# Kernel tuning notes

Measured on AMD Instinct MI355X. Metric: run time of the kernel, lower is better.

## Reference

```python
import jax, jax.numpy as jnp
import numpy as np

B = 128          # batch size
N_KG = 500       # KG vertices
N = N_KG + 2     # + sensor node + zero target node
D = 1024         # embed_dim (hard-coded in forward)
H = 256          # gnn_hidden
E = 4000         # edges
EPS = 1e-5


def setup_inputs() -> dict:
    key = jax.random.key(0)
    ks = jax.random.split(key, 8)
    return {
        "sensor_batch": jax.random.normal(ks[0], (B, D), jnp.float32),
        "base_vertices": jax.random.normal(ks[1], (N_KG, D), jnp.float32),
        "edge_index": jax.random.randint(ks[2], (2, E), 0, N, jnp.int64),
        "W1": jax.random.normal(ks[3], (D, H), jnp.float32) * (1.0 / np.sqrt(D)),
        "b1": jnp.zeros((H,), jnp.float32),
        "gamma1": jnp.ones((H,), jnp.float32),
        "beta1": jnp.zeros((H,), jnp.float32),
        "W2": jax.random.normal(ks[4], (H, H), jnp.float32) * (1.0 / np.sqrt(H)),
        "b2": jnp.zeros((H,), jnp.float32),
        "gamma2": jnp.ones((H,), jnp.float32),
        "beta2": jnp.zeros((H,), jnp.float32),
        "W3": jax.random.normal(ks[5], (H, H), jnp.float32) * (1.0 / np.sqrt(H)),
        "b3": jnp.zeros((H,), jnp.float32),
        "gamma3": jnp.ones((H,), jnp.float32),
        "beta3": jnp.zeros((H,), jnp.float32),
    }


def _gcn_norm(edge_index):
    # add self loops, symmetric normalization D^{-1/2} A D^{-1/2}
    loops = jnp.arange(N, dtype=edge_index.dtype)
    src = jnp.concatenate([edge_index[0], loops])
    dst = jnp.concatenate([edge_index[1], loops])
    deg = jnp.zeros((N,), jnp.float32).at[dst].add(1.0)
    dinv = jnp.where(deg > 0, jax.lax.rsqrt(deg), 0.0)
    norm = dinv[src] * dinv[dst]   # [E+N]
    return src, dst, norm


def _gcn_conv(x, W, b, src, dst, norm):
    # x: [B, N, F_in] -> [B, N, F_out]
    h = jnp.einsum('bnf,fh->bnh', x, W)
    msg = h[:, src, :] * norm[None, :, None]            # gather + scale
    out = jnp.zeros_like(h).at[:, dst, :].add(msg)      # scatter-add
    return out + b


def _bn_elu(x, gamma, beta):
    # BatchNorm1d over flattened (B*N, H) in training mode, then ELU
    Bn, Nn, Hh = x.shape
    xf = x.reshape(Bn * Nn, Hh)
    mean = jnp.mean(xf, axis=0)
    var = jnp.mean(jnp.square(xf - mean), axis=0)  # biased, as in torch BN fwd
    y = (xf - mean) * jax.lax.rsqrt(var + EPS) * gamma + beta
    return jax.nn.elu(y).reshape(Bn, Nn, Hh)


def reference(sensor_batch, base_vertices, edge_index,
              W1, b1, gamma1, beta1,
              W2, b2, gamma2, beta2,
              W3, b3, gamma3, beta3):
    Bn = sensor_batch.shape[0]
    # x = [base_vertices; sensor_input; zeros] per batch element -> [B, N, D]
    base = jnp.broadcast_to(base_vertices[None], (Bn, N_KG, D))
    zeros = jnp.zeros((Bn, 1, D), sensor_batch.dtype)
    x = jnp.concatenate([base, sensor_batch[:, None, :], zeros], axis=1)

    src, dst, norm = _gcn_norm(edge_index)
    x = _bn_elu(_gcn_conv(x, W1, b1, src, dst, norm), gamma1, beta1)
    x = _bn_elu(_gcn_conv(x, W2, b2, src, dst, norm), gamma2, beta2)
    x = _bn_elu(_gcn_conv(x, W3, b3, src, dst, norm), gamma3, beta3)
    return x
```

## Files before the change

kernel.cpp:

```cpp
#include <hip/hip_runtime.h>
#include <cstdint>
#include <cstddef>

#define NNODES 502
#define NKG    500
#define NPAD   512
#define NEDGE  4000
#define NET    4502
#define BB     128
#define DD     1024
#define HH     256
#define MROWS  (BB*NNODES)
#define MT     65536
#define MCAT   628
#define EPITCH 136

typedef short short8 __attribute__((ext_vector_type(8)));
typedef float f32x4  __attribute__((ext_vector_type(4)));

__device__ __forceinline__ unsigned short f2bf(float f) {
  union { float f; unsigned int u; } v; v.f = f;
  unsigned int r = v.u + 0x7fffu + ((v.u >> 16) & 1u);
  return (unsigned short)(r >> 16);
}

__device__ __forceinline__ float bf2f(unsigned short u) {
  union { unsigned int u; float f; } v; v.u = ((unsigned int)u) << 16;
  return v.f;
}

__device__ __forceinline__ float elu(float y) {
  return (y > 0.f) ? y : (__expf(y) - 1.f);
}

__device__ __forceinline__ void stage16(const void* g, void* l) {
  __builtin_amdgcn_global_load_lds((__attribute__((address_space(1))) void*)g,
                                   (__attribute__((address_space(3))) void*)l, 16, 0, 0);
}

__device__ __forceinline__ void mfma16(f32x4& c, short8 a, short8 b) {
  asm volatile("v_mfma_f32_16x16x32_bf16 %0, %1, %2, %0" : "+v"(c) : "v"(a), "v"(b));
}

__device__ inline void get_edge(const int* __restrict__ e, int i, int i64mode,
                                int& src, int& dst) {
  if (i < NEDGE) {
    if (i64mode) { src = e[2*i]; dst = e[2*NEDGE + 2*i]; }
    else         { src = e[i];   dst = e[NEDGE + i]; }
  } else {
    src = dst = i - NEDGE;
  }
  src = min(max(src, 0), NNODES-1);
  dst = min(max(dst, 0), NNODES-1);
}

__device__ __forceinline__ int detect_mode(const int* __restrict__ e) {
  __shared__ int sflag;
  if (threadIdx.x == 0) sflag = 0;
  __syncthreads();
  if (e[2*threadIdx.x + 1] != 0) atomicOr(&sflag, 1);
  __syncthreads();
  return sflag == 0;
}

__global__ void deg_kernel(const int* __restrict__ e, int* __restrict__ deg) {
  int i64 = detect_mode(e);
  int i = blockIdx.x*256 + threadIdx.x;
  if (i >= NET) return;
  int src, dst; get_edge(e, i, i64, src, dst);
  atomicAdd(&deg[dst], 1);
}

__global__ void scan_kernel(const int* __restrict__ deg, float* __restrict__ dinv,
                            int* __restrict__ rp, int* __restrict__ cursor) {
  __shared__ int s[512];
  int t = threadIdx.x;
  int cnt = (t < NNODES) ? deg[t] : 0;
  s[t] = cnt;
  if (t < NNODES) dinv[t] = rsqrtf((float)cnt);
  __syncthreads();
  for (int off = 1; off < 512; off <<= 1) {
    int v = (t >= off) ? s[t-off] : 0;
    __syncthreads();
    s[t] += v;
    __syncthreads();
  }
  if (t == 0) rp[0] = 0;
  if (t < NNODES) { rp[t+1] = s[t]; cursor[t] = s[t] - cnt; }
}

__global__ void fillsdf_kernel(const int* __restrict__ e, const float* __restrict__ dinv,
                               int* __restrict__ cursor, int* __restrict__ colA,
                               float* __restrict__ valA, float* __restrict__ Sdf) {
  int i64 = detect_mode(e);
  int i = blockIdx.x*256 + threadIdx.x;
  if (i >= NET) return;
  int src, dst; get_edge(e, i, i64, src, dst);
  float v = dinv[src] * dinv[dst];
  int pos = atomicAdd(&cursor[dst], 1);
  colA[pos] = src;
  valA[pos] = v;
  atomicAdd(&Sdf[dst*NPAD + src], v);
}

__global__ void sdcvt_kernel(const float* __restrict__ Sdf, unsigned short* __restrict__ Sd) {
  int i = blockIdx.x*256 + threadIdx.x;
  Sd[i] = f2bf(Sdf[i]);
}

__global__ __launch_bounds__(256) void prep_kernel(
    const float* __restrict__ W1, const float* __restrict__ W2, const float* __restrict__ W3,
    const float* __restrict__ base, const float* __restrict__ sensor,
    unsigned short* __restrict__ Wt1, unsigned short* __restrict__ Wt2,
    unsigned short* __restrict__ Wt3, unsigned short* __restrict__ Xp1,
    float* __restrict__ hcatz) {
  int bid = blockIdx.x, tid = threadIdx.x;
  if (bid < 512) {
    const float* W = (bid & 256) ? W3 : W2;
    unsigned short* Wt = (bid & 256) ? Wt3 : Wt2;
    int n = bid & 255;
    Wt[n*HH + tid] = f2bf(W[(size_t)tid*HH + n]);
  } else if (bid < 768) {
    int n = bid - 512;
    for (int k = tid; k < DD; k += 256)
      Wt1[n*DD + k] = f2bf(W1[(size_t)k*HH + n]);
  } else if (bid < 1408) {
    int i = (bid - 768)*256 + tid;
    int r = i >> 8, c = (i & 255) * 4;
    float4 v = make_float4(0.f, 0.f, 0.f, 0.f);
    if (r < NKG) v = *(const float4*)&base[(size_t)r*DD + c];
    else if (r < MCAT) v = *(const float4*)&sensor[(size_t)(r-NKG)*DD + c];
    union { unsigned short u[4]; uint2 d; } p;
    p.u[0]=f2bf(v.x); p.u[1]=f2bf(v.y); p.u[2]=f2bf(v.z); p.u[3]=f2bf(v.w);
    *(uint2*)&Xp1[(size_t)r*DD + c] = p.d;
  } else {
    hcatz[(bid - 1408)*256 + tid] = 0.f;
  }
}

__global__ __launch_bounds__(256) void gemm1m_kernel(
    const unsigned short* __restrict__ Ag,
    const unsigned short* __restrict__ Bg,
    float* __restrict__ C) {
  __shared__ unsigned short As[128*32];
  __shared__ unsigned short Bs[128*32];
  int tid = threadIdx.x;
  int wave = tid >> 6, lane = tid & 63;
  int l15 = lane & 15, quad = lane >> 4;
  int wm = (wave & 1) * 64, wn = (wave >> 1) * 64;
  int row0 = blockIdx.y * 128, col0 = blockIdx.x * 128;
  int kbase = blockIdx.z * 256;
  f32x4 acc[4][4] = {};
  for (int k0 = kbase; k0 < kbase + 256; k0 += 32) {
#pragma unroll
    for (int q = 0; q < 2; ++q) {
      int c = wave*128 + q*64 + lane;
      stage16(Ag + (size_t)(row0 + (c>>2))*DD + k0 + (c&3)*8, As + c*8);
      stage16(Bg + (size_t)(col0 + (c>>2))*DD + k0 + (c&3)*8, Bs + c*8);
    }
    __syncthreads();
    short8 af[4], bfv[4];
#pragma unroll
    for (int i = 0; i < 4; ++i) {
      af[i]  = *(const short8*)(As + (wm + i*16 + l15)*32 + quad*8);
      bfv[i] = *(const short8*)(Bs + (wn + i*16 + l15)*32 + quad*8);
    }
#pragma unroll
    for (int mi = 0; mi < 4; ++mi)
#pragma unroll
      for (int ni = 0; ni < 4; ++ni)
        mfma16(acc[mi][ni], af[mi], bfv[ni]);
    __syncthreads();
  }
  asm volatile("s_nop 7\n\ts_nop 7" ::);
#pragma unroll
  for (int ni = 0; ni < 4; ++ni) {
    int n = col0 + wn + ni*16 + l15;
#pragma unroll
    for (int mi = 0; mi < 4; ++mi) {
      int m = row0 + wm + mi*16 + quad*4;
#pragma unroll
      for (int r = 0; r < 4; ++r)
        if (m + r < MCAT) atomicAdd(&C[(size_t)(m+r)*HH + n], acc[mi][ni][r]);
    }
  }
}

__global__ void ac_kernel(const int* __restrict__ rp, const int* __restrict__ colA,
                          const float* __restrict__ valA, const float* __restrict__ hcat,
                          float* __restrict__ Abuf, float* __restrict__ cbuf) {
  int n = blockIdx.x, h = threadIdx.x;
  int s = rp[n], e = rp[n+1];
  float acc = 0.f, cacc = 0.f;
  for (int t = s; t < e; ++t) {
    int cl = colA[t]; float v = valA[t];
    if (cl < NKG) acc += v * hcat[cl*HH + h];
    else if (cl == NKG) cacc += v;
  }
  Abuf[n*HH + h] = acc;
  if (h == 0) cbuf[n] = cacc;
}

__global__ __launch_bounds__(256) void bn1n_kernel(
    const float* __restrict__ Abuf, const float* __restrict__ cbuf,
    const float* __restrict__ hcat,
    float* __restrict__ sA1, float* __restrict__ sAA1, float* __restrict__ sAc1,
    float* __restrict__ scp, float* __restrict__ ssA, float* __restrict__ sssA) {
  int bid = blockIdx.x, h = threadIdx.x;
  if (bid < 32) {
    int n0 = bid*16, n1 = min(n0+16, NNODES);
    float sA = 0, sAA = 0, sAc = 0, sc = 0, scc = 0;
    for (int n = n0; n < n1; ++n) {
      float a = Abuf[n*HH + h]; float cn = cbuf[n];
      sA += a; sAA += a*a; sAc += a*cn; sc += cn; scc += cn*cn;
    }
    atomicAdd(&sA1[h], sA); atomicAdd(&sAA1[h], sAA); atomicAdd(&sAc1[h], sAc);
    if (h == 0) { atomicAdd(&scp[0], sc); atomicAdd(&scp[1], scc); }
  } else {
    int b0 = (bid-32)*16;
    float ss = 0, sss = 0;
    for (int b = b0; b < b0+16; ++b) {
      float v = hcat[(size_t)(NKG + b)*HH + h]; ss += v; sss += v*v;
    }
    atomicAdd(&ssA[h], ss); atomicAdd(&sssA[h], sss);
  }
}

__global__ void fin1_kernel(const float* __restrict__ sA1, const float* __restrict__ sAA1,
                            const float* __restrict__ sAc1, const float* __restrict__ scp,
                            const float* __restrict__ ssA, const float* __restrict__ sssA,
                            const float* __restrict__ gamma, const float* __restrict__ beta,
                            float* __restrict__ scale, float* __restrict__ shift) {
  int h = threadIdx.x;
  float sA = sA1[h], sAA = sAA1[h], sAc = sAc1[h];
  float sc = scp[0], scc = scp[1];
  float ss = ssA[h], sss = sssA[h];
  const float cnt = (float)MROWS;
  float mean = ((float)BB * sA + sc*ss) / cnt;
  float msq  = ((float)BB * sAA + 2.f*sAc*ss + scc*sss) / cnt;
  float var  = msq - mean*mean;
  float scl  = gamma[h] * rsqrtf(var + 1e-5f);
  scale[h] = scl; shift[h] = beta[h] - mean*scl;
}

__global__ __launch_bounds__(256) void x2_kernel(
    const float* __restrict__ Abuf, const float* __restrict__ cbuf,
    const float* __restrict__ hcat, const float* __restrict__ scale,
    const float* __restrict__ shift, unsigned short* __restrict__ Xb) {
  int idx = blockIdx.x*256 + threadIdx.x;
  int row = idx >> 6, h0 = (idx & 63)*4;
  int b = row >> 9, n = row & (NPAD-1);
  union { unsigned short u[4]; uint2 d; } p;
  p.d = make_uint2(0,0);
  if (n < NNODES) {
    float4 a  = *(const float4*)(Abuf + n*HH + h0);
    float4 s  = *(const float4*)(hcat + (size_t)(NKG + b)*HH + h0);
    float4 sc = *(const float4*)(scale + h0);
    float4 sh = *(const float4*)(shift + h0);
    float cn = cbuf[n];
    p.u[0] = f2bf(elu((a.x + cn*s.x)*sc.x + sh.x));
    p.u[1] = f2bf(elu((a.y + cn*s.y)*sc.y + sh.y));
    p.u[2] = f2bf(elu((a.z + cn*s.z)*sc.z + sh.z));
    p.u[3] = f2bf(elu((a.w + cn*s.w)*sc.w + sh.w));
  }
  *(uint2*)(Xb + (size_t)row*HH + h0) = p.d;
}

template<int FBN>
__global__ __launch_bounds__(256) void gemmT3_kernel(
    const unsigned short* __restrict__ Ag,
    const unsigned short* __restrict__ Bg,
    const float* __restrict__ sums, const float* __restrict__ ssqs,
    const float* __restrict__ gamma, const float* __restrict__ beta,
    unsigned short* __restrict__ Tt) {
  __shared__ __align__(16) unsigned short smem[36864];
  __shared__ float sclL[256], shfL[256];
  unsigned short* As = smem;
  unsigned short* Bs = smem + 12288;
  int tid = threadIdx.x;
  int wave = tid >> 6, lane = tid & 63;
  int l15 = lane & 15, quad = lane >> 4;
  int wm = (wave & 1) * 64;
  int wnh = wave >> 1;
  int row0 = blockIdx.x * 128;
  if (FBN) {
    float mean = sums[tid] * (1.f/(float)MROWS);
    float var  = ssqs[tid] * (1.f/(float)MROWS) - mean*mean;
    float s = gamma[tid] * rsqrtf(var + 1e-5f);
    sclL[tid] = s; shfL[tid] = beta[tid] - mean*s;
    __syncthreads();
  }
  int c0 = tid, c1 = 256 + tid;
  int r0 = c0 >> 2, o0 = (c0 & 3) * 8;
  int r1 = c1 >> 2, o1 = (c1 & 3) * 8;
  const unsigned short* A0 = Ag + (size_t)(row0 + r0)*HH + o0;
  const unsigned short* A1 = Ag + (size_t)(row0 + r1)*HH + o1;

  auto XF = [&](uint4 v, int kk) -> uint4 {
    union { unsigned short u[8]; uint4 d; } va, pa;
    va.d = v;
#pragma unroll
    for (int s = 0; s < 8; ++s)
      pa.u[s] = f2bf(elu(bf2f(va.u[s])*sclL[kk+s] + shfL[kk+s]));
    return pa.d;
  };
  auto STAGE_B = [&](int kn, int buf) {
#pragma unroll
    for (int q = 0; q < 4; ++q) {
      int c = q*256 + tid;
      int rr = c >> 2, j = (c & 3)*8;
      stage16(Bg + (size_t)rr*HH + kn + j, Bs + buf*8192 + c*8);
    }
  };

  f32x4 acc[4][8] = {};
  if (FBN) {
    uint4 p00 = *(const uint4*)(A0);
    uint4 p01 = *(const uint4*)(A1);
    uint4 p10 = *(const uint4*)(A0 + 32);
    uint4 p11 = *(const uint4*)(A1 + 32);
    STAGE_B(0, 0);
    STAGE_B(32, 1);
    *(uint4*)(As + c0*8)        = XF(p00, o0);
    *(uint4*)(As + c1*8)        = XF(p01, o1);
    *(uint4*)(As + 4096 + c0*8) = XF(p10, 32 + o0);
    *(uint4*)(As + 4096 + c1*8) = XF(p11, 32 + o1);
    asm volatile("s_waitcnt lgkmcnt(0)" ::: "memory");
  } else {
    stage16(A0, As + c0*8);
    stage16(A1, As + c1*8);
    STAGE_B(0, 0);
    stage16(A0 + 32, As + 4096 + c0*8);
    stage16(A1 + 32, As + 4096 + c1*8);
    STAGE_B(32, 1);
  }
  uint4 na0, na1;
#pragma unroll
  for (int t = 0; t < 8; ++t) {
    int cur = t % 3;
    int nxt2 = (t + 2) % 3;
    if (FBN) {
      if (t >= 1 && t <= 6) {
        na0 = *(const uint4*)(A0 + (t+1)*32);
        na1 = *(const uint4*)(A1 + (t+1)*32);
      }
      if (t < 6) STAGE_B((t+2)*32, nxt2);
      if (t == 0)      asm volatile("s_waitcnt vmcnt(8)"  ::: "memory");
      else if (t <= 5) asm volatile("s_waitcnt vmcnt(10)" ::: "memory");
      else if (t == 6) asm volatile("s_waitcnt vmcnt(6)"  ::: "memory");
      else             asm volatile("s_waitcnt vmcnt(0)"  ::: "memory");
    } else {
      if (t < 6) {
        stage16(A0 + (t+2)*32, As + nxt2*4096 + c0*8);
        stage16(A1 + (t+2)*32, As + nxt2*4096 + c1*8);
        STAGE_B((t+2)*32, nxt2);
        asm volatile("s_waitcnt vmcnt(12)" ::: "memory");
      } else if (t == 6) {
        asm volatile("s_waitcnt vmcnt(6)" ::: "memory");
      } else {
        asm volatile("s_waitcnt vmcnt(0)" ::: "memory");
      }
    }
    __builtin_amdgcn_s_barrier();
    __builtin_amdgcn_sched_barrier(0);
    short8 af[4], bfv[8];
#pragma unroll
    for (int i = 0; i < 4; ++i)
      af[i] = *(const short8*)(As + cur*4096 + (wm + i*16 + l15)*32 + quad*8);
#pragma unroll
    for (int i = 0; i < 8; ++i)
      bfv[i] = *(const short8*)(Bs + cur*8192 + (wnh*128 + i*16 + l15)*32 + quad*8);
#pragma unroll
    for (int mi = 0; mi < 4; ++mi)
#pragma unroll
      for (int ni = 0; ni < 8; ++ni)
        mfma16(acc[mi][ni], af[mi], bfv[ni]);
    if (FBN && t >= 1 && t <= 6) {
      int nb = (t + 1) % 3;
      int kk = (t + 1) * 32;
      *(uint4*)(As + nb*4096 + c0*8) = XF(na0, kk + o0);
      *(uint4*)(As + nb*4096 + c1*8) = XF(na1, kk + o1);
      asm volatile("s_waitcnt lgkmcnt(0)" ::: "memory");
    }
    __builtin_amdgcn_sched_barrier(0);
    __builtin_amdgcn_s_barrier();
  }
  asm volatile("s_nop 7\n\ts_nop 7" ::);
  int moff = (tid & 15)*8;
#pragma unroll
  for (int nh = 0; nh < 2; ++nh) {
    if (wnh == nh) {
#pragma unroll
      for (int ni = 0; ni < 8; ++ni) {
        int nl = ni*16 + l15;
#pragma unroll
        for (int mi = 0; mi < 4; ++mi) {
          int ml = wm + mi*16 + quad*4;
#pragma unroll
          for (int r = 0; r < 4; ++r)
            smem[nl*EPITCH + ml + r] = f2bf(acc[mi][ni][r]);
        }
      }
    }
    __syncthreads();
#pragma unroll
    for (int j = 0; j < 8; ++j) {
      int nr = (tid >> 4) + j*16;
      uint4 d = *(const uint4*)(smem + nr*EPITCH + moff);
      *(uint4*)(Tt + (size_t)(nh*128 + nr)*MT + row0 + moff) = d;
    }
    __syncthreads();
  }
}

__global__ __launch_bounds__(256) void gemmS2_kernel(
    const unsigned short* __restrict__ Sd,
    const unsigned short* __restrict__ Tt,
    unsigned short* __restrict__ Xbo,
    float* __restrict__ sums, float* __restrict__ ssqs) {
  __shared__ __align__(16) unsigned short smem[36864];
  unsigned short* As = smem;
  unsigned short* Bs = smem + 12288;
  int tid = threadIdx.x;
  int wave = tid >> 6, lane = tid & 63;
  int l15 = lane & 15, quad = lane >> 4;
  int wm = (wave & 1) * 64, wn = (wave >> 1) * 64;
  int id = blockIdx.x;
  int xcd = id & 7;
  int w = id >> 3;
  int y = w & 3;
  int g = (w >> 2) * 8 + xcd;
  int x = g >> 6;
  int b = (g & 63) * 2;
  int row0 = y * 128, col0 = x * 128;
  const unsigned short* Abase = Sd + (size_t)row0*NPAD;
  const unsigned short* Bbase = Tt + (size_t)col0*MT + (size_t)b*NPAD;
  int c0 = tid, c1 = 256 + tid;
  int r0 = c0 >> 2, o0 = (c0 & 3) * 8;
  int r1 = c1 >> 2, o1 = (c1 & 3) * 8;

  f32x4 acc[2][4][4] = {};
  auto STAGE = [&](int kn, int buf) {
    stage16(Abase + (size_t)r0*NPAD + kn + o0, As + buf*4096 + c0*8);
    stage16(Abase + (size_t)r1*NPAD + kn + o1, As + buf*4096 + c1*8);
#pragma unroll
    for (int q = 0; q < 4; ++q) {
      int c = q*256 + tid;
      int bb = c >> 9, cc = c & 511;
      int rr = cc >> 2, j = (cc & 3)*8;
      stage16(Bbase + (size_t)rr*MT + bb*NPAD + kn + j, Bs + buf*8192 + c*8);
    }
  };
  STAGE(0, 0);
  STAGE(32, 1);
  for (int t = 0; t < 16; ++t) {
    int cur = t % 3;
    if (t < 14) {
      STAGE((t+2)*32, (t+2) % 3);
      asm volatile("s_waitcnt vmcnt(12)" ::: "memory");
    } else if (t == 14) {
      asm volatile("s_waitcnt vmcnt(6)" ::: "memory");
    } else {
      asm volatile("s_waitcnt vmcnt(0)" ::: "memory");
    }
    __builtin_amdgcn_s_barrier();
    __builtin_amdgcn_sched_barrier(0);
    short8 af[4], bfv[2][4];
#pragma unroll
    for (int i = 0; i < 4; ++i)
      af[i] = *(const short8*)(As + cur*4096 + (wm + i*16 + l15)*32 + quad*8);
#pragma unroll
    for (int bb = 0; bb < 2; ++bb)
#pragma unroll
      for (int i = 0; i < 4; ++i)
        bfv[bb][i] = *(const short8*)(Bs + cur*8192 + bb*4096 + (wn + i*16 + l15)*32 + quad*8);
#pragma unroll
    for (int bb = 0; bb < 2; ++bb)
#pragma unroll
      for (int mi = 0; mi < 4; ++mi)
#pragma unroll
        for (int ni = 0; ni < 4; ++ni)
          mfma16(acc[bb][mi][ni], af[mi], bfv[bb][ni]);
    __builtin_amdgcn_sched_barrier(0);
    __builtin_amdgcn_s_barrier();
  }
  asm volatile("s_nop 7\n\ts_nop 7" ::);
  float ps[4] = {0,0,0,0}, pq[4] = {0,0,0,0};
#pragma unroll
  for (int bb = 0; bb < 2; ++bb)
#pragma unroll
    for (int ni = 0; ni < 4; ++ni)
#pragma unroll
      for (int mi = 0; mi < 4; ++mi)
#pragma unroll
        for (int r = 0; r < 4; ++r) {
          float v = acc[bb][mi][ni][r];
          ps[ni] += v; pq[ni] += v*v;
        }
  int noff = (tid & 15)*8;
#pragma unroll
  for (int bb = 0; bb < 2; ++bb) {
#pragma unroll
    for (int mi = 0; mi < 4; ++mi) {
      int ml = wm + mi*16 + quad*4;
#pragma unroll
      for (int ni = 0; ni < 4; ++ni) {
        int nl = wn + ni*16 + l15;
#pragma unroll
        for (int r = 0; r < 4; ++r)
          smem[(ml + r)*EPITCH + nl] = f2bf(acc[bb][mi][ni][r]);
      }
    }
    __syncthreads();
    unsigned short* Xrow = Xbo + (size_t)(b + bb)*NPAD*HH;
#pragma unroll
    for (int j = 0; j < 8; ++j) {
      int rr = (tid >> 4) + j*16;
      int node = row0 + rr;
      if (node < NNODES) {
        uint4 d = *(const uint4*)(smem + rr*EPITCH + noff);
        *(uint4*)(Xrow + (size_t)node*HH + col0 + noff) = d;
      }
    }
    __syncthreads();
  }
  float* red = (float*)smem;
  red[tid] = 0.f;
  __syncthreads();
#pragma unroll
  for (int ni = 0; ni < 4; ++ni) {
    int cl = wn + ni*16 + l15;
    atomicAdd(&red[cl], ps[ni]);
    atomicAdd(&red[128+cl], pq[ni]);
  }
  __syncthreads();
  if (tid < 128) atomicAdd(&sums[col0+tid], red[tid]);
  else atomicAdd(&ssqs[col0+tid-128], red[tid]);
}

__global__ void finalize_kernel(const float* __restrict__ sums, const float* __restrict__ ssqs,
                                const float* __restrict__ gamma, const float* __restrict__ beta,
                                float* __restrict__ scale, float* __restrict__ shift) {
  int h = threadIdx.x;
  const float cnt = (float)MROWS;
  float mean = sums[h] / cnt;
  float var  = ssqs[h] / cnt - mean*mean;
  float scl  = gamma[h] * rsqrtf(var + 1e-5f);
  scale[h] = scl; shift[h] = beta[h] - mean*scl;
}

__global__ __launch_bounds__(256) void bnout_kernel(
    const unsigned short* __restrict__ Xb, const float* __restrict__ scale,
    const float* __restrict__ shift, float* __restrict__ O) {
  int idx = blockIdx.x*256 + threadIdx.x;
  int row = idx >> 6, h0 = (idx & 63)*4;
  int b = row >> 9, n = row & (NPAD-1);
  if (n >= NNODES) return;
  union { unsigned short u[4]; uint2 d; } v;
  v.d = *(const uint2*)(Xb + (size_t)row*HH + h0);
  float4 sc = *(const float4*)(scale + h0);
  float4 sh = *(const float4*)(shift + h0);
  float4 o;
  o.x = elu(bf2f(v.u[0])*sc.x + sh.x);
  o.y = elu(bf2f(v.u[1])*sc.y + sh.y);
  o.z = elu(bf2f(v.u[2])*sc.z + sh.z);
  o.w = elu(bf2f(v.u[3])*sc.w + sh.w);
  *(float4*)(O + ((size_t)(b*NNODES + n)*HH + h0)) = o;
}

extern "C" void kernel_launch(void* const* d_in, const int* in_sizes, int n_in,
                              void* d_out, int out_size, void* d_ws, size_t ws_size,
                              hipStream_t stream) {
  const float* sensor = (const float*)d_in[0];
  const float* base   = (const float*)d_in[1];
  const int*   eidx   = (const int*)d_in[2];
  const float* W1 = (const float*)d_in[3];
  const float* g1 = (const float*)d_in[5];
  const float* be1= (const float*)d_in[6];
  const float* W2 = (const float*)d_in[7];
  const float* g2 = (const float*)d_in[9];
  const float* be2= (const float*)d_in[10];
  const float* W3 = (const float*)d_in[11];
  const float* g3 = (const float*)d_in[13];
  const float* be3= (const float*)d_in[14];

  char* ws = (char*)d_ws;
  int*   deg    = (int*)(ws + 0);
  float* sum2   = (float*)(ws + 2048);
  float* ssq2   = (float*)(ws + 3072);
  float* sum3   = (float*)(ws + 4096);
  float* ssq3   = (float*)(ws + 5120);
  float* cbuf   = (float*)(ws + 6144);
  int*   cursor = (int*)(ws + 8192);
  float* sA1    = (float*)(ws + 10496);
  float* sAA1   = (float*)(ws + 11520);
  float* sAc1   = (float*)(ws + 12544);
  float* scp    = (float*)(ws + 13568);
  float* ssA    = (float*)(ws + 13824);
  float* sssA   = (float*)(ws + 14848);
  float* dinv   = (float*)(ws + 16384);
  int*   rp     = (int*)(ws + 18432);
  int*   colA   = (int*)(ws + 20480);
  float* valA   = (float*)(ws + 40960);
  float* scale1 = (float*)(ws + 61440);
  float* shift1 = (float*)(ws + 62464);
  float* scale3 = (float*)(ws + 65536);
  float* shift3 = (float*)(ws + 66560);
  float* Abuf   = (float*)(ws + 67584);
  float* hcat   = (float*)(ws + 581632);
  unsigned short* Wt2 = (unsigned short*)(ws + 1224704);
  unsigned short* Wt3 = (unsigned short*)(ws + 1355776);
  unsigned short* Sd  = (unsigned short*)(ws + 1486848);
  unsigned short* Xb  = (unsigned short*)(ws + 2011136);
  unsigned short* Tt  = (unsigned short*)(ws + 35565568UL);
  unsigned short* Xp1 = (unsigned short*)(ws + 35565568UL);
  unsigned short* Wt1 = (unsigned short*)(ws + 35565568UL + 1310720);
  float* out = (float*)d_out;
  float* Sdf = (float*)d_out;

  hipMemsetAsync(ws, 0, 16384, stream);
  hipMemsetAsync(d_out, 0, NPAD*NPAD*4, stream);
  deg_kernel<<<(NET+255)/256, 256, 0, stream>>>(eidx, deg);
  scan_kernel<<<1, 512, 0, stream>>>(deg, dinv, rp, cursor);
  fillsdf_kernel<<<(NET+255)/256, 256, 0, stream>>>(eidx, dinv, cursor, colA, valA, Sdf);
  sdcvt_kernel<<<(NPAD*NPAD)/256, 256, 0, stream>>>(Sdf, Sd);
  prep_kernel<<<2036, 256, 0, stream>>>(W1, W2, W3, base, sensor, Wt1, Wt2, Wt3, Xp1, hcat);

  gemm1m_kernel<<<dim3(2, 5, 4), 256, 0, stream>>>(Xp1, Wt1, hcat);
  ac_kernel<<<NNODES, 256, 0, stream>>>(rp, colA, valA, hcat, Abuf, cbuf);
  bn1n_kernel<<<40, 256, 0, stream>>>(Abuf, cbuf, hcat, sA1, sAA1, sAc1, scp, ssA, sssA);
  fin1_kernel<<<1, 256, 0, stream>>>(sA1, sAA1, sAc1, scp, ssA, sssA, g1, be1, scale1, shift1);
  x2_kernel<<<(MT*64)/256, 256, 0, stream>>>(Abuf, cbuf, hcat, scale1, shift1, Xb);

  gemmT3_kernel<0><<<MT/128, 256, 0, stream>>>(Xb, Wt2, sum2, ssq2, g2, be2, Tt);
  gemmS2_kernel<<<512, 256, 0, stream>>>(Sd, Tt, Xb, sum2, ssq2);
  gemmT3_kernel<1><<<MT/128, 256, 0, stream>>>(Xb, Wt3, sum2, ssq2, g2, be2, Tt);
  gemmS2_kernel<<<512, 256, 0, stream>>>(Sd, Tt, Xb, sum3, ssq3);
  finalize_kernel<<<1, 256, 0, stream>>>(sum3, ssq3, g3, be3, scale3, shift3);
  bnout_kernel<<<(MT*64)/256, 256, 0, stream>>>(Xb, scale3, shift3, out);
}
```

Before: 289.0 us.

## Replace dense adjacency GEMM aggregation with sparse CSR gather kernel

The layer 2/3 aggregation switches from a dense bf16 512x512 normalized-adjacency matrix multiply (with a transposed H layout) to a CSR gather-accumulate kernel that reads neighbor rows of H directly. The dense adjacency build, its bf16 conversion and the related memset are dropped, and the feature GEMM now writes H row-major. This removes the dense GEMM's mostly-zero work, since there are only about 4500 nonzeros against 262k entries. The cost is irregular gathers, a 64-float per-thread accumulator that raises register pressure, and many shared-memory atomics for the BN statistics.

```diff
diff --git a/kernel.cpp b/kernel.cpp
--- a/kernel.cpp
+++ b/kernel.cpp
@@ -14,6 +14,7 @@
 #define MT     65536
 #define MCAT   628
 #define EPITCH 136
+#define EP2    264
 
 typedef short short8 __attribute__((ext_vector_type(8)));
 typedef float f32x4  __attribute__((ext_vector_type(4)));
@@ -89,23 +90,16 @@
   if (t < NNODES) { rp[t+1] = s[t]; cursor[t] = s[t] - cnt; }
 }
 
-__global__ void fillsdf_kernel(const int* __restrict__ e, const float* __restrict__ dinv,
-                               int* __restrict__ cursor, int* __restrict__ colA,
-                               float* __restrict__ valA, float* __restrict__ Sdf) {
+__global__ void fill_kernel(const int* __restrict__ e, const float* __restrict__ dinv,
+                            int* __restrict__ cursor, int* __restrict__ colA,
+                            float* __restrict__ valA) {
   int i64 = detect_mode(e);
   int i = blockIdx.x*256 + threadIdx.x;
   if (i >= NET) return;
   int src, dst; get_edge(e, i, i64, src, dst);
-  float v = dinv[src] * dinv[dst];
   int pos = atomicAdd(&cursor[dst], 1);
   colA[pos] = src;
-  valA[pos] = v;
-  atomicAdd(&Sdf[dst*NPAD + src], v);
-}
-
-__global__ void sdcvt_kernel(const float* __restrict__ Sdf, unsigned short* __restrict__ Sd) {
-  int i = blockIdx.x*256 + threadIdx.x;
-  Sd[i] = f2bf(Sdf[i]);
+  valA[pos] = dinv[src] * dinv[dst];
 }
 
 __global__ __launch_bounds__(256) void prep_kernel(
@@ -272,7 +266,7 @@
     const unsigned short* __restrict__ Bg,
     const float* __restrict__ sums, const float* __restrict__ ssqs,
     const float* __restrict__ gamma, const float* __restrict__ beta,
-    unsigned short* __restrict__ Tt) {
+    unsigned short* __restrict__ Hout) {
   __shared__ __align__(16) unsigned short smem[36864];
   __shared__ float sclL[256], shfL[256];
   unsigned short* As = smem;
@@ -386,156 +380,96 @@
     __builtin_amdgcn_s_barrier();
   }
   asm volatile("s_nop 7\n\ts_nop 7" ::);
-  int moff = (tid & 15)*8;
-#pragma unroll
-  for (int nh = 0; nh < 2; ++nh) {
-    if (wnh == nh) {
-#pragma unroll
-      for (int ni = 0; ni < 8; ++ni) {
-        int nl = ni*16 + l15;
-#pragma unroll
-        for (int mi = 0; mi < 4; ++mi) {
-          int ml = wm + mi*16 + quad*4;
-#pragma unroll
-          for (int r = 0; r < 4; ++r)
-            smem[nl*EPITCH + ml + r] = f2bf(acc[mi][ni][r]);
-        }
-      }
-    }
-    __syncthreads();
-#pragma unroll
-    for (int j = 0; j < 8; ++j) {
-      int nr = (tid >> 4) + j*16;
-      uint4 d = *(const uint4*)(smem + nr*EPITCH + moff);
-      *(uint4*)(Tt + (size_t)(nh*128 + nr)*MT + row0 + moff) = d;
-    }
-    __syncthreads();
-  }
-}
-
-__global__ __launch_bounds__(256) void gemmS2_kernel(
-    const unsigned short* __restrict__ Sd,
-    const unsigned short* __restrict__ Tt,
+#pragma unroll
+  for (int ni = 0; ni < 8; ++ni) {
+    int nl = wnh*128 + ni*16 + l15;
+#pragma unroll
+    for (int mi = 0; mi < 4; ++mi) {
+      int ml = wm + mi*16 + quad*4;
+#pragma unroll
+      for (int r = 0; r < 4; ++r)
+        smem[(ml + r)*EP2 + nl] = f2bf(acc[mi][ni][r]);
+    }
+  }
+  __syncthreads();
+  int colq = (tid & 31) * 8;
+  int rbase = tid >> 5;
+#pragma unroll
+  for (int j = 0; j < 16; ++j) {
+    int row = j*8 + rbase;
+    uint4 d = *(const uint4*)(smem + row*EP2 + colq);
+    *(uint4*)(Hout + (size_t)(row0 + row)*HH + colq) = d;
+  }
+}
+
+__global__ __launch_bounds__(256) void agg_kernel(
+    const int* __restrict__ rp, const int* __restrict__ colA,
+    const float* __restrict__ valA, const unsigned short* __restrict__ H,
     unsigned short* __restrict__ Xbo,
     float* __restrict__ sums, float* __restrict__ ssqs) {
-  __shared__ __align__(16) unsigned short smem[36864];
-  unsigned short* As = smem;
-  unsigned short* Bs = smem + 12288;
+  __shared__ float red[512];
+  int id = blockIdx.x;
+  int b = id & 127, chunk = id >> 7;
   int tid = threadIdx.x;
-  int wave = tid >> 6, lane = tid & 63;
-  int l15 = lane & 15, quad = lane >> 4;
-  int wm = (wave & 1) * 64, wn = (wave >> 1) * 64;
-  int id = blockIdx.x;
-  int xcd = id & 7;
-  int w = id >> 3;
-  int y = w & 3;
-  int g = (w >> 2) * 8 + xcd;
-  int x = g >> 6;
-  int b = (g & 63) * 2;
-  int row0 = y * 128, col0 = x * 128;
-  const unsigned short* Abase = Sd + (size_t)row0*NPAD;
-  const unsigned short* Bbase = Tt + (size_t)col0*MT + (size_t)b*NPAD;
-  int c0 = tid, c1 = 256 + tid;
-  int r0 = c0 >> 2, o0 = (c0 & 3) * 8;
-  int r1 = c1 >> 2, o1 = (c1 & 3) * 8;
-
-  f32x4 acc[2][4][4] = {};
-  auto STAGE = [&](int kn, int buf) {
-    stage16(Abase + (size_t)r0*NPAD + kn + o0, As + buf*4096 + c0*8);
-    stage16(Abase + (size_t)r1*NPAD + kn + o1, As + buf*4096 + c1*8);
-#pragma unroll
-    for (int q = 0; q < 4; ++q) {
-      int c = q*256 + tid;
-      int bb = c >> 9, cc = c & 511;
-      int rr = cc >> 2, j = (cc & 3)*8;
-      stage16(Bbase + (size_t)rr*MT + bb*NPAD + kn + j, Bs + buf*8192 + c*8);
-    }
-  };
-  STAGE(0, 0);
-  STAGE(32, 1);
-  for (int t = 0; t < 16; ++t) {
-    int cur = t % 3;
-    if (t < 14) {
-      STAGE((t+2)*32, (t+2) % 3);
-      asm volatile("s_waitcnt vmcnt(12)" ::: "memory");
-    } else if (t == 14) {
-      asm volatile("s_waitcnt vmcnt(6)" ::: "memory");
-    } else {
-      asm volatile("s_waitcnt vmcnt(0)" ::: "memory");
-    }
-    __builtin_amdgcn_s_barrier();
-    __builtin_amdgcn_sched_barrier(0);
-    short8 af[4], bfv[2][4];
-#pragma unroll
-    for (int i = 0; i < 4; ++i)
-      af[i] = *(const short8*)(As + cur*4096 + (wm + i*16 + l15)*32 + quad*8);
-#pragma unroll
-    for (int bb = 0; bb < 2; ++bb)
-#pragma unroll
-      for (int i = 0; i < 4; ++i)
-        bfv[bb][i] = *(const short8*)(Bs + cur*8192 + bb*4096 + (wn + i*16 + l15)*32 + quad*8);
-#pragma unroll
-    for (int bb = 0; bb < 2; ++bb)
-#pragma unroll
-      for (int mi = 0; mi < 4; ++mi)
-#pragma unroll
-        for (int ni = 0; ni < 4; ++ni)
-          mfma16(acc[bb][mi][ni], af[mi], bfv[bb][ni]);
-    __builtin_amdgcn_sched_barrier(0);
-    __builtin_amdgcn_s_barrier();
-  }
-  asm volatile("s_nop 7\n\ts_nop 7" ::);
-  float ps[4] = {0,0,0,0}, pq[4] = {0,0,0,0};
-#pragma unroll
-  for (int bb = 0; bb < 2; ++bb)
-#pragma unroll
-    for (int ni = 0; ni < 4; ++ni)
-#pragma unroll
-      for (int mi = 0; mi < 4; ++mi)
-#pragma unroll
-        for (int r = 0; r < 4; ++r) {
-          float v = acc[bb][mi][ni][r];
-          ps[ni] += v; pq[ni] += v*v;
-        }
-  int noff = (tid & 15)*8;
-#pragma unroll
-  for (int bb = 0; bb < 2; ++bb) {
-#pragma unroll
-    for (int mi = 0; mi < 4; ++mi) {
-      int ml = wm + mi*16 + quad*4;
-#pragma unroll
-      for (int ni = 0; ni < 4; ++ni) {
-        int nl = wn + ni*16 + l15;
-#pragma unroll
-        for (int r = 0; r < 4; ++r)
-          smem[(ml + r)*EPITCH + nl] = f2bf(acc[bb][mi][ni][r]);
+  int dst = chunk*64 + (tid >> 2);
+  int c0 = (tid & 3) * 64;
+  float acc[64];
+#pragma unroll
+  for (int j = 0; j < 64; ++j) acc[j] = 0.f;
+  const unsigned short* Hb = H + (size_t)b*NPAD*HH + c0;
+  if (dst < NNODES) {
+    int s = rp[dst], e = rp[dst+1];
+    int t = s;
+    for (; t + 1 < e; t += 2) {
+      int s0 = colA[t], s1 = colA[t+1];
+      float v0 = valA[t], v1 = valA[t+1];
+      const unsigned short* r0 = Hb + (size_t)s0*HH;
+      const unsigned short* r1 = Hb + (size_t)s1*HH;
+      union { unsigned short u[8]; uint4 d; } w0[8], w1[8];
+#pragma unroll
+      for (int q = 0; q < 8; ++q) w0[q].d = *(const uint4*)(r0 + q*8);
+#pragma unroll
+      for (int q = 0; q < 8; ++q) w1[q].d = *(const uint4*)(r1 + q*8);
+#pragma unroll
+      for (int q = 0; q < 8; ++q)
+#pragma unroll
+        for (int j = 0; j < 8; ++j)
+          acc[q*8+j] += v0 * bf2f(w0[q].u[j]) + v1 * bf2f(w1[q].u[j]);
+    }
+    if (t < e) {
+      int s0 = colA[t]; float v0 = valA[t];
+      const unsigned short* r0 = Hb + (size_t)s0*HH;
+#pragma unroll
+      for (int q = 0; q < 8; ++q) {
+        union { unsigned short u[8]; uint4 d; } w;
+        w.d = *(const uint4*)(r0 + q*8);
+#pragma unroll
+        for (int j = 0; j < 8; ++j)
+          acc[q*8+j] += v0 * bf2f(w.u[j]);
       }
     }
-    __syncthreads();
-    unsigned short* Xrow = Xbo + (size_t)(b + bb)*NPAD*HH;
-#pragma unroll
-    for (int j = 0; j < 8; ++j) {
-      int rr = (tid >> 4) + j*16;
-      int node = row0 + rr;
-      if (node < NNODES) {
-        uint4 d = *(const uint4*)(smem + rr*EPITCH + noff);
-        *(uint4*)(Xrow + (size_t)node*HH + col0 + noff) = d;
-      }
-    }
-    __syncthreads();
-  }
-  float* red = (float*)smem;
-  red[tid] = 0.f;
+    unsigned short* orow = Xbo + (size_t)b*NPAD*HH + (size_t)dst*HH + c0;
+#pragma unroll
+    for (int q = 0; q < 8; ++q) {
+      union { unsigned short u[8]; uint4 d; } p;
+#pragma unroll
+      for (int j = 0; j < 8; ++j) p.u[j] = f2bf(acc[q*8+j]);
+      *(uint4*)(orow + q*8) = p.d;
+    }
+  }
+  red[tid] = 0.f; red[256 + tid] = 0.f;
   __syncthreads();
-#pragma unroll
-  for (int ni = 0; ni < 4; ++ni) {
-    int cl = wn + ni*16 + l15;
-    atomicAdd(&red[cl], ps[ni]);
-    atomicAdd(&red[128+cl], pq[ni]);
+  if (dst < NNODES) {
+#pragma unroll
+    for (int j = 0; j < 64; ++j) {
+      float v = acc[j];
+      atomicAdd(&red[c0 + j], v);
+      atomicAdd(&red[256 + c0 + j], v*v);
+    }
   }
   __syncthreads();
-  if (tid < 128) atomicAdd(&sums[col0+tid], red[tid]);
-  else atomicAdd(&ssqs[col0+tid-128], red[tid]);
+  atomicAdd(&sums[tid], red[tid]);
+  atomicAdd(&ssqs[tid], red[256 + tid]);
 }
 
 __global__ void finalize_kernel(const float* __restrict__ sums, const float* __restrict__ ssqs,
@@ -610,20 +544,16 @@
   float* hcat   = (float*)(ws + 581632);
   unsigned short* Wt2 = (unsigned short*)(ws + 1224704);
   unsigned short* Wt3 = (unsigned short*)(ws + 1355776);
-  unsigned short* Sd  = (unsigned short*)(ws + 1486848);
   unsigned short* Xb  = (unsigned short*)(ws + 2011136);
-  unsigned short* Tt  = (unsigned short*)(ws + 35565568UL);
+  unsigned short* Hbuf= (unsigned short*)(ws + 35565568UL);
   unsigned short* Xp1 = (unsigned short*)(ws + 35565568UL);
   unsigned short* Wt1 = (unsigned short*)(ws + 35565568UL + 1310720);
   float* out = (float*)d_out;
-  float* Sdf = (float*)d_out;
 
   hipMemsetAsync(ws, 0, 16384, stream);
-  hipMemsetAsync(d_out, 0, NPAD*NPAD*4, stream);
   deg_kernel<<<(NET+255)/256, 256, 0, stream>>>(eidx, deg);
   scan_kernel<<<1, 512, 0, stream>>>(deg, dinv, rp, cursor);
-  fillsdf_kernel<<<(NET+255)/256, 256, 0, stream>>>(eidx, dinv, cursor, colA, valA, Sdf);
-  sdcvt_kernel<<<(NPAD*NPAD)/256, 256, 0, stream>>>(Sdf, Sd);
+  fill_kernel<<<(NET+255)/256, 256, 0, stream>>>(eidx, dinv, cursor, colA, valA);
   prep_kernel<<<2036, 256, 0, stream>>>(W1, W2, W3, base, sensor, Wt1, Wt2, Wt3, Xp1, hcat);
 
   gemm1m_kernel<<<dim3(2, 5, 4), 256, 0, stream>>>(Xp1, Wt1, hcat);
@@ -632,10 +562,10 @@
   fin1_kernel<<<1, 256, 0, stream>>>(sA1, sAA1, sAc1, scp, ssA, sssA, g1, be1, scale1, shift1);
   x2_kernel<<<(MT*64)/256, 256, 0, stream>>>(Abuf, cbuf, hcat, scale1, shift1, Xb);
 
-  gemmT3_kernel<0><<<MT/128, 256, 0, stream>>>(Xb, Wt2, sum2, ssq2, g2, be2, Tt);
-  gemmS2_kernel<<<512, 256, 0, stream>>>(Sd, Tt, Xb, sum2, ssq2);
-  gemmT3_kernel<1><<<MT/128, 256, 0, stream>>>(Xb, Wt3, sum2, ssq2, g2, be2, Tt);
-  gemmS2_kernel<<<512, 256, 0, stream>>>(Sd, Tt, Xb, sum3, ssq3);
+  gemmT3_kernel<0><<<MT/128, 256, 0, stream>>>(Xb, Wt2, sum2, ssq2, g2, be2, Hbuf);
+  agg_kernel<<<1024, 256, 0, stream>>>(rp, colA, valA, Hbuf, Xb, sum2, ssq2);
+  gemmT3_kernel<1><<<MT/128, 256, 0, stream>>>(Xb, Wt3, sum2, ssq2, g2, be2, Hbuf);
+  agg_kernel<<<1024, 256, 0, stream>>>(rp, colA, valA, Hbuf, Xb, sum3, ssq3);
   finalize_kernel<<<1, 256, 0, stream>>>(sum3, ssq3, g3, be3, scale3, shift3);
   bnout_kernel<<<(MT*64)/256, 256, 0, stream>>>(Xb, scale3, shift3, out);
 }
```

After: 685.6 us. 2.37x slower.
